# Optimization experiments

Hardware: AMD Instinct MI355X
Metric: run time of the kernel (lower is better)

Reference implementation:

```python
import jax, jax.numpy as jnp
import numpy as np

B, T, C, H = 2, 2048, 1024, 16
D = C // H  # d_head = 64
SCALE = 1.0 / float(np.sqrt(D))


def setup_inputs() -> dict:
    key = jax.random.key(0)
    ks = jax.random.split(key, 9)
    s = 0.02  # small init so softmax isn't fully saturated
    inp = {
        "x": jax.random.normal(ks[0], (B, T, C), jnp.float32),
        # causal mask, broadcast over batch and heads; mask==0 positions are blocked
        "mask": jnp.tril(jnp.ones((T, T), jnp.int32))[None, None, :, :],
        "wq": jax.random.normal(ks[1], (C, C), jnp.float32) * s,
        "bq": jnp.zeros((C,), jnp.float32),
        "wk": jax.random.normal(ks[2], (C, C), jnp.float32) * s,
        "bk": jnp.zeros((C,), jnp.float32),
        "wv": jax.random.normal(ks[3], (C, C), jnp.float32) * s,
        "bv": jnp.zeros((C,), jnp.float32),
        "wo": jax.random.normal(ks[4], (C, C), jnp.float32) * s,
        "bo": jnp.zeros((C,), jnp.float32),
    }
    return inp


def reference(x, mask, wq, bq, wk, bk, wv, bv, wo, bo):
    Bx, Tx, Cx = x.shape
    # torch nn.Linear: y = x @ W.T + b
    def lin(z, w, b):
        return jnp.einsum("btc,oc->bto", z, w) + b

    def split_heads(z):  # [B,T,C] -> [B,H,T,D]
        return z.reshape(Bx, Tx, H, D).transpose(0, 2, 1, 3)

    q = split_heads(lin(x, wq, bq))
    k = split_heads(lin(x, wk, bk))
    v = split_heads(lin(x, wv, bv))

    scores = jnp.einsum("bhqd,bhkd->bhqk", q, k) * SCALE  # [B,H,T,T]
    scores = jnp.where(mask == 0, jnp.float32(-1e9), scores)
    probs = jax.nn.softmax(scores, axis=-1)

    # post-softmax entropy statistic (full T x T materialization, as in source)
    entropy = -(probs * jnp.log(probs + 1e-9)).sum(-1).mean()

    out = jnp.einsum("bhqk,bhkd->bhqd", probs, v)  # [B,H,T,D]
    out = out.transpose(0, 2, 1, 3).reshape(Bx, Tx, Cx)
    out = jnp.einsum("btc,oc->bto", out, wo) + bo
    return out, entropy
```

## Files before the change

### kernel.cpp

```cpp
#include <hip/hip_runtime.h>
#include <math.h>

typedef short bf8_t __attribute__((ext_vector_type(8)));
typedef float f4_t  __attribute__((ext_vector_type(4)));
typedef unsigned int u32;
typedef unsigned short u16;

#define MFMA(a,b,c) __builtin_amdgcn_mfma_f32_16x16x32_bf16((a),(b),(c),0,0,0)

__device__ __forceinline__ void gload16(const void* g, void* l) {
  __builtin_amdgcn_global_load_lds(
      (const __attribute__((address_space(1))) void*)g,
      (__attribute__((address_space(3))) void*)l, 16, 0, 0);
}

__device__ __forceinline__ u16 f2bf(float f) {
  u32 u = __float_as_uint(f);
  u += 0x7fff + ((u >> 16) & 1);
  return (u16)(u >> 16);
}

__device__ __forceinline__ u32 cvtpk(float a, float b) {
  u32 r;
  asm("v_cvt_pk_bf16_f32 %0, %1, %2" : "=v"(r) : "v"(a), "v"(b));
  return r;
}

__device__ __forceinline__ void gemm_tile(
    const u16* __restrict__ A, const u16* __restrict__ Bm,
    int lda, int ldb, int m0, int n0, int K,
    short* smem, f4_t acc[4][4], int tid)
{
  const int lane = tid & 63, w = tid >> 6;
  const int lo = lane & 15, hi = lane >> 4;
  const int wr = (w >> 1) * 64, wc = (w & 1) * 64;
  const int nsteps = K >> 6;

  auto STAGE = [&](int step, int buf) {
    int k0 = step * 64;
#pragma unroll
    for (int iss = 0; iss < 4; ++iss) {
      int bb = iss * 4096 + tid * 16;
      int row = bb >> 7;
      int lg = ((bb >> 4) & 7) ^ (row & 7);
      gload16(A  + (size_t)(m0 + row) * lda + k0 + lg * 8,
              (char*)smem + buf * 16384 + iss * 4096 + w * 1024);
      gload16(Bm + (size_t)(n0 + row) * ldb + k0 + lg * 8,
              (char*)smem + 32768 + buf * 16384 + iss * 4096 + w * 1024);
    }
  };

  STAGE(0, 0);
  int cur = 0;
  for (int step = 0; step < nsteps; ++step) {
    if (step + 1 < nsteps) {
      STAGE(step + 1, cur ^ 1);
      asm volatile("s_waitcnt vmcnt(8)\n\ts_barrier" ::: "memory");
    } else {
      asm volatile("s_waitcnt vmcnt(0)\n\ts_barrier" ::: "memory");
    }
    const short* As = (const short*)((char*)smem + cur * 16384);
    const short* Bs = (const short*)((char*)smem + 32768 + cur * 16384);
#pragma unroll
    for (int kk = 0; kk < 2; ++kk) {
      bf8_t af[4], bfr[4];
#pragma unroll
      for (int m = 0; m < 4; ++m) {
        int row = wr + m * 16 + lo;
        int g = (kk * 4 + hi) ^ (row & 7);
        af[m] = *(const bf8_t*)&As[row * 64 + g * 8];
      }
#pragma unroll
      for (int n = 0; n < 4; ++n) {
        int row = wc + n * 16 + lo;
        int g = (kk * 4 + hi) ^ (row & 7);
        bfr[n] = *(const bf8_t*)&Bs[row * 64 + g * 8];
      }
#pragma unroll
      for (int m = 0; m < 4; ++m)
#pragma unroll
        for (int n = 0; n < 4; ++n)
          acc[m][n] = MFMA(af[m], bfr[n], acc[m][n]);
    }
    asm volatile("s_barrier" ::: "memory");
    cur ^= 1;
  }
}

__global__ __launch_bounds__(256)
void convert_kernel(const float* __restrict__ x,  const float* __restrict__ wq,
                    const float* __restrict__ wk, const float* __restrict__ wv,
                    const float* __restrict__ wo,
                    u16* xb, u16* wqb, u16* wkb, u16* wvb, u16* wob, float* ent)
{
  size_t i = (size_t)blockIdx.x * 256 + threadIdx.x;
  if (blockIdx.x == 0 && threadIdx.x == 0) *ent = 0.f;
  const float* src; u16* dst; size_t off;
  if (i < 524288) { src = x; dst = xb; off = i; }
  else {
    size_t r = i - 524288;
    int sel = (int)(r >> 17);
    off = r & 131071;
    src = sel == 0 ? wq : sel == 1 ? wk : sel == 2 ? wv : wo;
    dst = sel == 0 ? wqb : sel == 1 ? wkb : sel == 2 ? wvb : wob;
  }
  f4_t a = *(const f4_t*)&src[off * 8];
  f4_t c = *(const f4_t*)&src[off * 8 + 4];
  u16 t[8] = {f2bf(a[0]), f2bf(a[1]), f2bf(a[2]), f2bf(a[3]),
              f2bf(c[0]), f2bf(c[1]), f2bf(c[2]), f2bf(c[3])};
  *(uint4*)&dst[off * 8] = *(const uint4*)t;
}

__global__ __launch_bounds__(256)
void qkv_kernel(const u16* __restrict__ X, const u16* __restrict__ Wq,
                const u16* __restrict__ Wk, const u16* __restrict__ Wv,
                const float* __restrict__ bq, const float* __restrict__ bk,
                const float* __restrict__ bv,
                u16* Qo, u16* Ko, u16* Vto)
{
  __shared__ short smem[32768];
  const int tid = threadIdx.x;
  const int nb = blockIdx.x;
  const int which = nb >> 3;
  const int n0 = (nb & 7) * 128;
  const int m0 = blockIdx.y * 128;
  const u16* W    = which == 0 ? Wq : which == 1 ? Wk : Wv;
  const float* bias = which == 0 ? bq : which == 1 ? bk : bv;

  f4_t acc[4][4];
#pragma unroll
  for (int m = 0; m < 4; ++m)
#pragma unroll
    for (int n = 0; n < 4; ++n) acc[m][n] = f4_t{0.f, 0.f, 0.f, 0.f};

  gemm_tile(X, W, 1024, 1024, m0, n0, 1024, smem, acc, tid);

  const int lane = tid & 63, w = tid >> 6;
  const int lo = lane & 15, hi = lane >> 4;
  const int wr = (w >> 1) * 64, wc = (w & 1) * 64;
  const float scl = (which == 0) ? 0.125f : 1.0f;
  char* ep = (char*)smem;
  const int bix = m0 >> 11, t0g = m0 & 2047;

  if (which < 2) {
#pragma unroll
    for (int n = 0; n < 4; ++n) {
      int c = wc + n * 16 + lo;
      float bb = bias[n0 + c];
#pragma unroll
      for (int m = 0; m < 4; ++m)
#pragma unroll
        for (int j = 0; j < 4; ++j) {
          int r = wr + m * 16 + hi * 4 + j;
          int pg = (c >> 3) ^ ((r & 7) << 1);
          *(u16*)(ep + r * 256 + pg * 16 + (c & 7) * 2) =
              f2bf((acc[m][n][j] + bb) * scl);
        }
    }
    __syncthreads();
    u16* Out = (which == 0) ? Qo : Ko;
#pragma unroll
    for (int rep = 0; rep < 8; ++rep) {
      int r = rep * 16 + (tid >> 4);
      int seg = tid & 15;
      int pg = seg ^ ((r & 7) << 1);
      uint4 v = *(uint4*)(ep + r * 256 + pg * 16);
      int hh = (n0 >> 6) + (seg >> 3);
      int d = (seg & 7) * 8;
      *(uint4*)&Out[(((size_t)bix * 16 + hh) * 2048 + t0g + r) * 64 + d] = v;
    }
  } else {
#pragma unroll
    for (int n = 0; n < 4; ++n) {
      int c = wc + n * 16 + lo;
      float bb = bias[n0 + c];
#pragma unroll
      for (int m = 0; m < 4; ++m)
#pragma unroll
        for (int jp = 0; jp < 2; ++jp) {
          int r = wr + m * 16 + hi * 4 + jp * 2;
          u32 pk = cvtpk(acc[m][n][jp * 2] + bb, acc[m][n][jp * 2 + 1] + bb);
          int pg = (r >> 3) ^ ((c & 7) << 1);
          *(u32*)(ep + c * 256 + pg * 16 + (r & 7) * 2) = pk;
        }
    }
    __syncthreads();
#pragma unroll
    for (int rep = 0; rep < 8; ++rep) {
      int c = rep * 16 + (tid >> 4);
      int seg = tid & 15;
      int pg = seg ^ ((c & 7) << 1);
      uint4 v = *(uint4*)(ep + c * 256 + pg * 16);
      int f = n0 + c;
      int hh = f >> 6, d = f & 63;
      *(uint4*)&Vto[(((size_t)bix * 16 + hh) * 64 + d) * 2048 + t0g + seg * 8] = v;
    }
  }
}

__global__ __launch_bounds__(256, 4)
void attn_kernel(const u16* __restrict__ Qg, const u16* __restrict__ Kg,
                 const u16* __restrict__ Vtg, u16* __restrict__ Att,
                 float* __restrict__ Ent)
{
  __shared__ char smem[40960];
  const int tid = threadIdx.x, lane = tid & 63, w = tid >> 6;
  const int lo = lane & 15, hi = lane >> 4;
  const int n = blockIdx.x;
  const int bh = (n & 7) * 4 + ((n >> 3) & 3);
  const int p = n >> 5;
  const int b = bh >> 4, h = bh & 15;
  const u16* Qb  = Qg  + (size_t)bh * (2048 * 64);
  const u16* Kb  = Kg  + (size_t)bh * (2048 * 64);
  const u16* Vtb = Vtg + (size_t)bh * (64 * 2048);
  u16* Attp = Att + (size_t)b * (2048 * 1024) + h * 64;
  short* Pw = (short*)(smem + 32768 + w * 2048);

  auto STAGE = [&](int kt, int buf) {
#pragma unroll
    for (int iss = 0; iss < 2; ++iss) {
      int bb = iss * 4096 + tid * 16;
      int row = bb >> 7;
      int lg = ((bb >> 4) & 7) ^ (row & 7);
      gload16(Kb + (size_t)(kt * 64 + row) * 64 + lg * 8,
              smem + buf * 8192 + iss * 4096 + w * 1024);
      gload16(Vtb + (size_t)row * 2048 + kt * 64 + lg * 8,
              smem + 16384 + buf * 8192 + iss * 4096 + w * 1024);
    }
  };

  float hs_total = 0.f;

  for (int ph = 0; ph < 2; ++ph) {
    const int g = ph ? (31 - p) : p;
    const int q0 = g * 64;
    const int nt = g + 1;
    const int qrow = q0 + w * 16 + lo;

    bf8_t qf[2];
#pragma unroll
    for (int kk = 0; kk < 2; ++kk)
      qf[kk] = *(const bf8_t*)&Qb[(size_t)qrow * 64 + kk * 32 + hi * 8];

    f4_t o[4];
#pragma unroll
    for (int md = 0; md < 4; ++md) o[md] = f4_t{0.f, 0.f, 0.f, 0.f};
    float m_ = -3.0e38f, l_ = 0.f, E_ = 0.f;

    STAGE(0, 0);
    int cur = 0;

    for (int kt = 0; kt < nt; ++kt) {
      if (kt + 1 < nt) {
        STAGE(kt + 1, cur ^ 1);
        asm volatile("s_waitcnt vmcnt(4)\n\ts_barrier" ::: "memory");
      } else {
        asm volatile("s_waitcnt vmcnt(0)\n\ts_barrier" ::: "memory");
      }
      const short* KL = (const short*)(smem + cur * 8192);
      const short* VL = (const short*)(smem + 16384 + cur * 8192);

      f4_t s[4];
#pragma unroll
      for (int mk = 0; mk < 4; ++mk) s[mk] = f4_t{0.f, 0.f, 0.f, 0.f};
#pragma unroll
      for (int kk = 0; kk < 2; ++kk) {
        bf8_t kf[4];
#pragma unroll
        for (int mk = 0; mk < 4; ++mk) {
          int row = mk * 16 + lo;
          int gg = (kk * 4 + hi) ^ (row & 7);
          kf[mk] = *(const bf8_t*)&KL[row * 64 + gg * 8];
        }
#pragma unroll
        for (int mk = 0; mk < 4; ++mk)
          s[mk] = MFMA(kf[mk], qf[kk], s[mk]);
      }

      if (kt == nt - 1) {
#pragma unroll
        for (int mk = 0; mk < 4; ++mk)
#pragma unroll
          for (int jj = 0; jj < 4; ++jj)
            if ((mk * 16 + hi * 4 + jj) > (w * 16 + lo)) s[mk][jj] = -1.0e30f;
      }

      float mt = s[0][0];
#pragma unroll
      for (int mk = 0; mk < 4; ++mk)
#pragma unroll
        for (int jj = 0; jj < 4; ++jj) mt = fmaxf(mt, s[mk][jj]);
      mt = fmaxf(mt, __shfl_xor(mt, 16));
      mt = fmaxf(mt, __shfl_xor(mt, 32));
      if (!__all(mt <= m_ + 8.f)) {
        float mnew = fmaxf(m_, mt);
        float f = __expf(m_ - mnew);
        l_ *= f; E_ *= f;
#pragma unroll
        for (int md = 0; md < 4; ++md) o[md] *= f;
        m_ = mnew;
      }
      float pv16[16];
#pragma unroll
      for (int mk = 0; mk < 4; ++mk)
#pragma unroll
        for (int jj = 0; jj < 4; ++jj) {
          float pv = __expf(s[mk][jj] - m_);
          pv16[mk * 4 + jj] = pv;
          l_ += pv; E_ += pv * s[mk][jj];
        }

#pragma unroll
      for (int mk = 0; mk < 4; ++mk) {
        u32 a = cvtpk(pv16[mk * 4 + 0], pv16[mk * 4 + 1]);
        u32 c = cvtpk(pv16[mk * 4 + 2], pv16[mk * 4 + 3]);
        int gg = (mk * 2 + (hi >> 1)) ^ (lo & 7);
        *(uint2*)&Pw[lo * 64 + gg * 8 + (hi & 1) * 4] = make_uint2(a, c);
      }

#pragma unroll
      for (int kh = 0; kh < 2; ++kh) {
        int gp = (kh * 4 + hi) ^ (lo & 7);
        bf8_t pf = *(const bf8_t*)&Pw[lo * 64 + gp * 8];
#pragma unroll
        for (int md = 0; md < 4; ++md) {
          int row = md * 16 + lo;
          int gv = (kh * 4 + hi) ^ (row & 7);
          bf8_t vf = *(const bf8_t*)&VL[row * 64 + gv * 8];
          o[md] = MFMA(vf, pf, o[md]);
        }
      }
      asm volatile("s_barrier" ::: "memory");
      cur ^= 1;
    }

    l_ += __shfl_xor(l_, 16); l_ += __shfl_xor(l_, 32);
    E_ += __shfl_xor(E_, 16); E_ += __shfl_xor(E_, 32);

    float invl = 1.0f / l_;
#pragma unroll
    for (int md = 0; md < 4; ++md) {
      u32 w0 = cvtpk(o[md][0] * invl, o[md][1] * invl);
      u32 w1 = cvtpk(o[md][2] * invl, o[md][3] * invl);
      *(uint2*)&Attp[(size_t)qrow * 1024 + md * 16 + hi * 4] =
          make_uint2(w0, w1);
    }
    hs_total += (hi == 0) ? (m_ + __logf(l_) - E_ * invl) : 0.f;
  }

  float hs = hs_total;
#pragma unroll
  for (int off = 1; off < 64; off <<= 1) hs += __shfl_xor(hs, off);
  if (lane == 0) atomicAdd(Ent, hs * (1.0f / 65536.0f));
}

__global__ __launch_bounds__(256)
void proj_kernel(const u16* __restrict__ Attb, const u16* __restrict__ Wo,
                 const float* __restrict__ bo, float* __restrict__ Out)
{
  __shared__ short smem[32768];
  const int tid = threadIdx.x;
  const int n0 = blockIdx.x * 128;
  const int m0 = blockIdx.y * 128;

  f4_t acc[4][4];
#pragma unroll
  for (int m = 0; m < 4; ++m)
#pragma unroll
    for (int n = 0; n < 4; ++n) acc[m][n] = f4_t{0.f, 0.f, 0.f, 0.f};

  gemm_tile(Attb, Wo, 1024, 1024, m0, n0, 1024, smem, acc, tid);

  const int lane = tid & 63, w = tid >> 6;
  const int lo = lane & 15, hi = lane >> 4;
  const int wc = (w & 1) * 64;
  float* ep = (float*)smem;

#pragma unroll
  for (int pass = 0; pass < 2; ++pass) {
    __syncthreads();
    if ((w >> 1) == pass) {
#pragma unroll
      for (int n = 0; n < 4; ++n) {
        int c = wc + n * 16 + lo;
        float bb = bo[n0 + c];
#pragma unroll
        for (int m = 0; m < 4; ++m)
#pragma unroll
          for (int j = 0; j < 4; ++j) {
            int r = m * 16 + hi * 4 + j;
            int pg = (c >> 2) ^ ((r & 7) << 2);
            ep[r * 128 + pg * 4 + (c & 3)] = acc[m][n][j] + bb;
          }
      }
    }
    __syncthreads();
    int r = tid >> 2, q = tid & 3;
#pragma unroll
    for (int i = 0; i < 8; ++i) {
      int g = q * 8 + i;
      int pg = g ^ ((r & 7) << 2);
      f4_t v = *(f4_t*)&ep[r * 128 + pg * 4];
      *(f4_t*)&Out[(size_t)(m0 + pass * 64 + r) * 1024 + n0 + g * 4] = v;
    }
  }
}

extern "C" void kernel_launch(void* const* d_in, const int* in_sizes, int n_in,
                              void* d_out, int out_size, void* d_ws, size_t ws_size,
                              hipStream_t stream)
{
  const float* x  = (const float*)d_in[0];
  const float* wq = (const float*)d_in[2];
  const float* bq = (const float*)d_in[3];
  const float* wk = (const float*)d_in[4];
  const float* bk = (const float*)d_in[5];
  const float* wv = (const float*)d_in[6];
  const float* bv = (const float*)d_in[7];
  const float* wo = (const float*)d_in[8];
  const float* bo = (const float*)d_in[9];

  float* out = (float*)d_out;
  float* ent = out + (size_t)2 * 2048 * 1024;

  char* ws = (char*)d_ws;
  u16* xb   = (u16*)ws;
  u16* wqb  = (u16*)(ws + 8388608);
  u16* wkb  = (u16*)(ws + 8388608 + 2097152);
  u16* wvb  = (u16*)(ws + 8388608 + 2 * 2097152);
  u16* wob  = (u16*)(ws + 8388608 + 3 * 2097152);
  u16* Qb   = (u16*)(ws + 16777216);
  u16* Kb   = (u16*)(ws + 16777216 + 8388608);
  u16* Vtb  = (u16*)(ws + 16777216 + 2 * 8388608);
  u16* Attb = (u16*)(ws + 16777216 + 3 * 8388608);

  convert_kernel<<<4096, 256, 0, stream>>>(x, wq, wk, wv, wo,
                                           xb, wqb, wkb, wvb, wob, ent);
  qkv_kernel<<<dim3(24, 32), 256, 0, stream>>>(xb, wqb, wkb, wvb,
                                               bq, bk, bv, Qb, Kb, Vtb);
  attn_kernel<<<512, 256, 0, stream>>>(Qb, Kb, Vtb, Attb, ent);
  proj_kernel<<<dim3(8, 32), 256, 0, stream>>>(Attb, wob, bo, out);
}
```

Before: 220.5 us.

## Process paired causal query tiles in one shared K/V loop

Each attention block used to run two separate passes over K/V, one for query tile p and one for tile 31-p. It now streams K/V tiles once and computes both query tiles on each staged tile. The low tile is masked off after its diagonal, so K/V global loads and LDS staging are roughly halved per block. The block-to-tile mapping is also interleaved to balance work across the grid. In exchange, register pressure and LDS use go up: the second P buffer raises shared memory to 48KB, which may lower occupancy. Synchronisation moves to __syncthreads at the end of each iteration, which waits for the prefetch to finish before the next tile.

```diff
diff --git a/kernel.cpp b/kernel.cpp
--- a/kernel.cpp
+++ b/kernel.cpp
@@ -203,18 +203,21 @@
                  const u16* __restrict__ Vtg, u16* __restrict__ Att,
                  float* __restrict__ Ent)
 {
-  __shared__ char smem[40960];
+  __shared__ char smem[49152];
   const int tid = threadIdx.x, lane = tid & 63, w = tid >> 6;
   const int lo = lane & 15, hi = lane >> 4;
   const int n = blockIdx.x;
   const int bh = (n & 7) * 4 + ((n >> 3) & 3);
-  const int p = n >> 5;
+  const int idx = n >> 5;
+  const int p = (idx < 8) ? 2 * idx : 15 - 2 * (idx - 8);
+  const int nt = 32 - p;
   const int b = bh >> 4, h = bh & 15;
   const u16* Qb  = Qg  + (size_t)bh * (2048 * 64);
   const u16* Kb  = Kg  + (size_t)bh * (2048 * 64);
   const u16* Vtb = Vtg + (size_t)bh * (64 * 2048);
   u16* Attp = Att + (size_t)b * (2048 * 1024) + h * 64;
-  short* Pw = (short*)(smem + 32768 + w * 2048);
+  short* PwA = (short*)(smem + 32768 + (w * 2 + 0) * 2048);
+  short* PwB = (short*)(smem + 32768 + (w * 2 + 1) * 2048);
 
   auto STAGE = [&](int kt, int buf) {
 #pragma unroll
@@ -229,114 +232,131 @@
     }
   };
 
-  float hs_total = 0.f;
-
-  for (int ph = 0; ph < 2; ++ph) {
-    const int g = ph ? (31 - p) : p;
-    const int q0 = g * 64;
-    const int nt = g + 1;
-    const int qrow = q0 + w * 16 + lo;
-
-    bf8_t qf[2];
-#pragma unroll
-    for (int kk = 0; kk < 2; ++kk)
-      qf[kk] = *(const bf8_t*)&Qb[(size_t)qrow * 64 + kk * 32 + hi * 8];
-
-    f4_t o[4];
-#pragma unroll
-    for (int md = 0; md < 4; ++md) o[md] = f4_t{0.f, 0.f, 0.f, 0.f};
-    float m_ = -3.0e38f, l_ = 0.f, E_ = 0.f;
-
-    STAGE(0, 0);
-    int cur = 0;
-
-    for (int kt = 0; kt < nt; ++kt) {
-      if (kt + 1 < nt) {
-        STAGE(kt + 1, cur ^ 1);
-        asm volatile("s_waitcnt vmcnt(4)\n\ts_barrier" ::: "memory");
-      } else {
-        asm volatile("s_waitcnt vmcnt(0)\n\ts_barrier" ::: "memory");
-      }
-      const short* KL = (const short*)(smem + cur * 8192);
-      const short* VL = (const short*)(smem + 16384 + cur * 8192);
-
-      f4_t s[4];
-#pragma unroll
-      for (int mk = 0; mk < 4; ++mk) s[mk] = f4_t{0.f, 0.f, 0.f, 0.f};
-#pragma unroll
-      for (int kk = 0; kk < 2; ++kk) {
-        bf8_t kf[4];
-#pragma unroll
-        for (int mk = 0; mk < 4; ++mk) {
-          int row = mk * 16 + lo;
-          int gg = (kk * 4 + hi) ^ (row & 7);
-          kf[mk] = *(const bf8_t*)&KL[row * 64 + gg * 8];
-        }
-#pragma unroll
-        for (int mk = 0; mk < 4; ++mk)
-          s[mk] = MFMA(kf[mk], qf[kk], s[mk]);
-      }
-
-      if (kt == nt - 1) {
-#pragma unroll
-        for (int mk = 0; mk < 4; ++mk)
-#pragma unroll
-          for (int jj = 0; jj < 4; ++jj)
-            if ((mk * 16 + hi * 4 + jj) > (w * 16 + lo)) s[mk][jj] = -1.0e30f;
-      }
-
-      float mt = s[0][0];
+  const int qrowA = p * 64 + w * 16 + lo;
+  const int qrowB = (31 - p) * 64 + w * 16 + lo;
+  bf8_t qfA[2], qfB[2];
+#pragma unroll
+  for (int kk = 0; kk < 2; ++kk) {
+    qfA[kk] = *(const bf8_t*)&Qb[(size_t)qrowA * 64 + kk * 32 + hi * 8];
+    qfB[kk] = *(const bf8_t*)&Qb[(size_t)qrowB * 64 + kk * 32 + hi * 8];
+  }
+
+  f4_t oA[4], oB[4];
+#pragma unroll
+  for (int md = 0; md < 4; ++md) {
+    oA[md] = f4_t{0.f, 0.f, 0.f, 0.f};
+    oB[md] = f4_t{0.f, 0.f, 0.f, 0.f};
+  }
+  float mA = -3.0e38f, lA = 0.f, EA = 0.f;
+  float mB = -3.0e38f, lB = 0.f, EB = 0.f;
+
+  auto sm_update = [&](f4_t (&s)[4], float& m_, float& l_, float& E_,
+                       f4_t (&o)[4], short* Pw) {
+    float mt = s[0][0];
+#pragma unroll
+    for (int mk = 0; mk < 4; ++mk)
+#pragma unroll
+      for (int jj = 0; jj < 4; ++jj) mt = fmaxf(mt, s[mk][jj]);
+    mt = fmaxf(mt, __shfl_xor(mt, 16));
+    mt = fmaxf(mt, __shfl_xor(mt, 32));
+    if (!__all(mt <= m_ + 8.f)) {
+      float mnew = fmaxf(m_, mt);
+      float f = __expf(m_ - mnew);
+      l_ *= f; E_ *= f;
+#pragma unroll
+      for (int md = 0; md < 4; ++md) o[md] *= f;
+      m_ = mnew;
+    }
+    float pv16[16];
+#pragma unroll
+    for (int mk = 0; mk < 4; ++mk)
+#pragma unroll
+      for (int jj = 0; jj < 4; ++jj) {
+        float pv = __expf(s[mk][jj] - m_);
+        pv16[mk * 4 + jj] = pv;
+        l_ += pv; E_ += pv * s[mk][jj];
+      }
+#pragma unroll
+    for (int mk = 0; mk < 4; ++mk) {
+      u32 a = cvtpk(pv16[mk * 4 + 0], pv16[mk * 4 + 1]);
+      u32 c = cvtpk(pv16[mk * 4 + 2], pv16[mk * 4 + 3]);
+      int gg = (mk * 2 + (hi >> 1)) ^ (lo & 7);
+      *(uint2*)&Pw[lo * 64 + gg * 8 + (hi & 1) * 4] = make_uint2(a, c);
+    }
+  };
+
+  STAGE(0, 0);
+  __syncthreads();
+  int cur = 0;
+
+  for (int kt = 0; kt < nt; ++kt) {
+    if (kt + 1 < nt) STAGE(kt + 1, cur ^ 1);
+    const short* KL = (const short*)(smem + cur * 8192);
+    const short* VL = (const short*)(smem + 16384 + cur * 8192);
+    const bool aAct = (kt <= p);
+
+    f4_t sA[4], sB[4];
+#pragma unroll
+    for (int mk = 0; mk < 4; ++mk) {
+      sA[mk] = f4_t{0.f, 0.f, 0.f, 0.f};
+      sB[mk] = f4_t{0.f, 0.f, 0.f, 0.f};
+    }
+#pragma unroll
+    for (int kk = 0; kk < 2; ++kk) {
+      bf8_t kf[4];
+#pragma unroll
+      for (int mk = 0; mk < 4; ++mk) {
+        int row = mk * 16 + lo;
+        int gg = (kk * 4 + hi) ^ (row & 7);
+        kf[mk] = *(const bf8_t*)&KL[row * 64 + gg * 8];
+      }
+#pragma unroll
+      for (int mk = 0; mk < 4; ++mk) {
+        sB[mk] = MFMA(kf[mk], qfB[kk], sB[mk]);
+        if (aAct) sA[mk] = MFMA(kf[mk], qfA[kk], sA[mk]);
+      }
+    }
+
+    if (kt == nt - 1) {
 #pragma unroll
       for (int mk = 0; mk < 4; ++mk)
 #pragma unroll
-        for (int jj = 0; jj < 4; ++jj) mt = fmaxf(mt, s[mk][jj]);
-      mt = fmaxf(mt, __shfl_xor(mt, 16));
-      mt = fmaxf(mt, __shfl_xor(mt, 32));
-      if (!__all(mt <= m_ + 8.f)) {
-        float mnew = fmaxf(m_, mt);
-        float f = __expf(m_ - mnew);
-        l_ *= f; E_ *= f;
-#pragma unroll
-        for (int md = 0; md < 4; ++md) o[md] *= f;
-        m_ = mnew;
-      }
-      float pv16[16];
+        for (int jj = 0; jj < 4; ++jj)
+          if ((mk * 16 + hi * 4 + jj) > (w * 16 + lo)) sB[mk][jj] = -1.0e30f;
+    }
+    if (aAct && kt == p) {
 #pragma unroll
       for (int mk = 0; mk < 4; ++mk)
 #pragma unroll
-        for (int jj = 0; jj < 4; ++jj) {
-          float pv = __expf(s[mk][jj] - m_);
-          pv16[mk * 4 + jj] = pv;
-          l_ += pv; E_ += pv * s[mk][jj];
-        }
-
-#pragma unroll
-      for (int mk = 0; mk < 4; ++mk) {
-        u32 a = cvtpk(pv16[mk * 4 + 0], pv16[mk * 4 + 1]);
-        u32 c = cvtpk(pv16[mk * 4 + 2], pv16[mk * 4 + 3]);
-        int gg = (mk * 2 + (hi >> 1)) ^ (lo & 7);
-        *(uint2*)&Pw[lo * 64 + gg * 8 + (hi & 1) * 4] = make_uint2(a, c);
-      }
-
-#pragma unroll
-      for (int kh = 0; kh < 2; ++kh) {
-        int gp = (kh * 4 + hi) ^ (lo & 7);
-        bf8_t pf = *(const bf8_t*)&Pw[lo * 64 + gp * 8];
-#pragma unroll
-        for (int md = 0; md < 4; ++md) {
-          int row = md * 16 + lo;
-          int gv = (kh * 4 + hi) ^ (row & 7);
-          bf8_t vf = *(const bf8_t*)&VL[row * 64 + gv * 8];
-          o[md] = MFMA(vf, pf, o[md]);
-        }
-      }
-      asm volatile("s_barrier" ::: "memory");
-      cur ^= 1;
-    }
-
+        for (int jj = 0; jj < 4; ++jj)
+          if ((mk * 16 + hi * 4 + jj) > (w * 16 + lo)) sA[mk][jj] = -1.0e30f;
+    }
+
+    sm_update(sB, mB, lB, EB, oB, PwB);
+    if (aAct) sm_update(sA, mA, lA, EA, oA, PwA);
+
+#pragma unroll
+    for (int kh = 0; kh < 2; ++kh) {
+      int gp = (kh * 4 + hi) ^ (lo & 7);
+      bf8_t pfB = *(const bf8_t*)&PwB[lo * 64 + gp * 8];
+      bf8_t pfA;
+      if (aAct) pfA = *(const bf8_t*)&PwA[lo * 64 + gp * 8];
+#pragma unroll
+      for (int md = 0; md < 4; ++md) {
+        int row = md * 16 + lo;
+        int gv = (kh * 4 + hi) ^ (row & 7);
+        bf8_t vf = *(const bf8_t*)&VL[row * 64 + gv * 8];
+        oB[md] = MFMA(vf, pfB, oB[md]);
+        if (aAct) oA[md] = MFMA(vf, pfA, oA[md]);
+      }
+    }
+    __syncthreads();
+    cur ^= 1;
+  }
+
+  auto epi = [&](float m_, float l_, float E_, f4_t (&o)[4], int qrow) {
     l_ += __shfl_xor(l_, 16); l_ += __shfl_xor(l_, 32);
     E_ += __shfl_xor(E_, 16); E_ += __shfl_xor(E_, 32);
-
     float invl = 1.0f / l_;
 #pragma unroll
     for (int md = 0; md < 4; ++md) {
@@ -345,10 +365,10 @@
       *(uint2*)&Attp[(size_t)qrow * 1024 + md * 16 + hi * 4] =
           make_uint2(w0, w1);
     }
-    hs_total += (hi == 0) ? (m_ + __logf(l_) - E_ * invl) : 0.f;
-  }
-
-  float hs = hs_total;
+    return (hi == 0) ? (m_ + __logf(l_) - E_ * invl) : 0.f;
+  };
+  float hs = epi(mB, lB, EB, oB, qrowB) + epi(mA, lA, EA, oA, qrowA);
+
 #pragma unroll
   for (int off = 1; off < 64; off <<= 1) hs += __shfl_xor(hs, off);
   if (lane == 0) atomicAdd(Ent, hs * (1.0f / 65536.0f));
```

Result: slower. 226.3 us (+2.6%).
